# Performance work log

Measured on AMD Instinct MI355X. Metric: run time of the kernel, lower is better.

## Reference

```python
import jax, jax.numpy as jnp
import numpy as np

B, C, N, M, S = 16384, 256, 128, 20, 3  # batch, controller dim, mem locations, mem vec size, shifts
EMIT = M + 1 + 1 + S + 1  # 26


def setup_inputs() -> dict:
    key = jax.random.key(0)
    k1, k2, k3, k4, k5 = jax.random.split(key, 5)
    controller_output = jax.random.normal(k1, (B, C), dtype=jnp.float32)
    w_t_prev = jax.random.uniform(k2, (B, N), dtype=jnp.float32)
    M_t = jax.random.normal(k3, (B, N, M), dtype=jnp.float32)
    # fc_addr dense params (glorot-ish scale)
    W_addr = jax.random.normal(k4, (C, EMIT), dtype=jnp.float32) * (1.0 / np.sqrt(C))
    b_addr = jax.random.normal(k5, (EMIT,), dtype=jnp.float32) * 0.01
    return {"controller_output": controller_output, "w_t_prev": w_t_prev,
            "M_t": M_t, "W_addr": W_addr, "b_addr": b_addr}


def reference(controller_output, w_t_prev, M_t, W_addr, b_addr):
    # fc_addr: Dense with tanh activation
    fc = jnp.tanh(controller_output @ W_addr + b_addr)  # [B, 26]
    k_t = fc[:, :M]                                      # [B, 20]
    beta_t = jax.nn.softplus(fc[:, M:M + 1])             # [B, 1]
    g_t = jax.nn.sigmoid(fc[:, M + 1:M + 2])             # [B, 1]
    s_t = jax.nn.softmax(fc[:, M + 2:M + 2 + S], axis=-1)  # [B, 3]
    gamma_t = 1.0 + jax.nn.softplus(fc[:, M + 2 + S:])   # [B, 1]

    # content addressing: cosine similarity (no epsilon, as in source)
    dot = jnp.einsum('bm,bnm->bn', k_t, M_t)             # [B, N]
    k_mag = jnp.sqrt(jnp.sum(k_t * k_t, axis=-1, keepdims=True))   # [B, 1]
    m_mag = jnp.sqrt(jnp.sum(M_t * M_t, axis=-1))                  # [B, N]
    w_c_t = jax.nn.softmax(beta_t * dot / (k_mag * m_mag), axis=-1)

    # interpolation
    w_g_t = g_t * w_c_t + (1.0 - g_t) * w_t_prev         # [B, N]

    # circular convolutional shift: w~[j] = sum_i s[i] * w_g[(j - (i - S//2)) % N]
    idx = (jnp.arange(N)[:, None] - (jnp.arange(S)[None, :] - S // 2)) % N  # [N, S]
    w_tilde = jnp.einsum('bns,bs->bn', w_g_t[:, idx], s_t)  # [B, N]

    # sharpening
    w_raised = jnp.power(w_tilde, gamma_t)
    w_t = w_raised / jnp.sum(w_raised, axis=-1, keepdims=True)
    return w_t
```

## Files before the change

kernel.cpp:

```cpp
#include <hip/hip_runtime.h>
#include <math.h>

#define B_    16384
#define C_    256
#define N_    128
#define M_    20
#define S_    3
#define EMIT_ 26

__global__ __launch_bounds__(256, 4) void ntm_wave2_kernel(
    const float* __restrict__ ctrl,
    const float* __restrict__ w_prev,
    const float* __restrict__ Mt,
    const float* __restrict__ W,
    const float* __restrict__ bvec,
    float* __restrict__ out)
{
    const int lane = threadIdx.x & 63;
    const int wid  = threadIdx.x >> 6;
    const int b    = blockIdx.x * 4 + wid;

    __shared__ float c_lds[4][C_];

    const float* M0 = Mt + ((size_t)b * N_ + lane) * M_;
    const float* M1 = M0 + (size_t)64 * M_;
    float4 ma[5], mb[5];
    #pragma unroll
    for (int i = 0; i < 5; ++i) ma[i] = *(const float4*)(M0 + 4 * i);
    #pragma unroll
    for (int i = 0; i < 5; ++i) mb[i] = *(const float4*)(M1 + 4 * i);
    const float wp0 = w_prev[(size_t)b * N_ + lane];
    const float wp1 = w_prev[(size_t)b * N_ + lane + 64];

    const float* crow = ctrl + (size_t)b * C_;
    {
        float4 cv = *(const float4*)(crow + lane * 4);
        *(float4*)&c_lds[wid][lane * 4] = cv;
    }

    const int jr = lane & 31;
    const int j  = (jr < EMIT_) ? jr : (EMIT_ - 1);
    const int q  = lane >> 5;
    const float* cq = &c_lds[wid][q * 128];
    const float* Wq = W + (size_t)(q * 128) * EMIT_ + j;
    float a0 = 0.f, a1 = 0.f;
    #pragma unroll 8
    for (int io = 0; io < 128; io += 2) {
        a0 = fmaf(cq[io],     Wq[(size_t)io * EMIT_],       a0);
        a1 = fmaf(cq[io + 1], Wq[(size_t)(io + 1) * EMIT_], a1);
    }
    float a = a0 + a1;
    a += __shfl_xor(a, 32);
    a = tanhf(a + bvec[j]);

    float fc[EMIT_];
    #pragma unroll
    for (int jj = 0; jj < EMIT_; ++jj) fc[jj] = __shfl(a, jj);

    float ksq = 0.f;
    #pragma unroll
    for (int m = 0; m < M_; ++m) ksq = fmaf(fc[m], fc[m], ksq);

    const float beta  = log1pf(__expf(fc[20]));
    const float g     = 1.f / (1.f + __expf(-fc[21]));
    const float e0 = __expf(fc[22]);
    const float e1 = __expf(fc[23]);
    const float e2 = __expf(fc[24]);
    const float einv = 1.f / (e0 + e1 + e2);
    const float s0 = e0 * einv, s1 = e1 * einv, s2 = e2 * einv;
    const float gamma = 1.f + log1pf(__expf(fc[25]));

    float dot0 = 0.f, msq0 = 0.f, dot1 = 0.f, msq1 = 0.f;
    #pragma unroll
    for (int i = 0; i < 5; ++i) {
        float4 v = ma[i];
        dot0 = fmaf(fc[4*i+0], v.x, dot0);  msq0 = fmaf(v.x, v.x, msq0);
        dot0 = fmaf(fc[4*i+1], v.y, dot0);  msq0 = fmaf(v.y, v.y, msq0);
        dot0 = fmaf(fc[4*i+2], v.z, dot0);  msq0 = fmaf(v.z, v.z, msq0);
        dot0 = fmaf(fc[4*i+3], v.w, dot0);  msq0 = fmaf(v.w, v.w, msq0);
    }
    #pragma unroll
    for (int i = 0; i < 5; ++i) {
        float4 v = mb[i];
        dot1 = fmaf(fc[4*i+0], v.x, dot1);  msq1 = fmaf(v.x, v.x, msq1);
        dot1 = fmaf(fc[4*i+1], v.y, dot1);  msq1 = fmaf(v.y, v.y, msq1);
        dot1 = fmaf(fc[4*i+2], v.z, dot1);  msq1 = fmaf(v.z, v.z, msq1);
        dot1 = fmaf(fc[4*i+3], v.w, dot1);  msq1 = fmaf(v.w, v.w, msq1);
    }
    const float l0 = beta * dot0 / sqrtf(ksq * msq0);
    const float l1 = beta * dot1 / sqrtf(ksq * msq1);

    float mx = fmaxf(l0, l1);
    #pragma unroll
    for (int o = 32; o; o >>= 1) mx = fmaxf(mx, __shfl_xor(mx, o));
    const float p0 = __expf(l0 - mx);
    const float p1 = __expf(l1 - mx);
    float sm = p0 + p1;
    #pragma unroll
    for (int o = 32; o; o >>= 1) sm += __shfl_xor(sm, o);
    const float inv_sm = 1.f / sm;

    const float A  = g * (p0 * inv_sm) + (1.f - g) * wp0;
    const float Bv = g * (p1 * inv_sm) + (1.f - g) * wp1;

    const float Ap  = __shfl(A,  (lane + 1) & 63);
    const float Bp  = __shfl(Bv, (lane + 1) & 63);
    const float Am  = __shfl(A,  (lane + 63) & 63);
    const float Bm  = __shfl(Bv, (lane + 63) & 63);
    const float A0  = __shfl(A, 0);
    const float A63 = __shfl(A, 63);
    const float B0  = __shfl(Bv, 0);
    const float B63 = __shfl(Bv, 63);

    const float np0 = (lane == 63) ? B0  : Ap;
    const float nm0 = (lane == 0)  ? B63 : Am;
    const float np1 = (lane == 63) ? A0  : Bp;
    const float nm1 = (lane == 0)  ? A63 : Bm;

    const float wt0 = np0 * s0 + A  * s1 + nm0 * s2;
    const float wt1 = np1 * s0 + Bv * s1 + nm1 * s2;

    const float wr0 = (wt0 > 0.f) ? __expf(gamma * __logf(wt0)) : 0.f;
    const float wr1 = (wt1 > 0.f) ? __expf(gamma * __logf(wt1)) : 0.f;
    float tot = wr0 + wr1;
    #pragma unroll
    for (int o = 32; o; o >>= 1) tot += __shfl_xor(tot, o);
    const float inv_tot = 1.f / tot;

    float* orow = out + (size_t)b * N_;
    orow[lane]      = wr0 * inv_tot;
    orow[lane + 64] = wr1 * inv_tot;
}

extern "C" void kernel_launch(void* const* d_in, const int* in_sizes, int n_in,
                              void* d_out, int out_size, void* d_ws, size_t ws_size,
                              hipStream_t stream) {
    const float* ctrl   = (const float*)d_in[0];
    const float* w_prev = (const float*)d_in[1];
    const float* Mt     = (const float*)d_in[2];
    const float* W      = (const float*)d_in[3];
    const float* bvec   = (const float*)d_in[4];
    float* out = (float*)d_out;

    ntm_wave2_kernel<<<dim3(B_ / 4), dim3(256), 0, stream>>>(ctrl, w_prev, Mt, W, bvec, out);
}
```

Baseline: 42.80 us.

## Restructure fc_addr matvec: 4-way K split, two outputs per lane, no LDS

The dense controller projection is re-partitioned so each lane computes two adjacent output columns over a 64-element slice of C, with four slices combined by shuffles. The LDS staging of the controller row is removed in favour of direct float4 loads, and W is read as float2. The projection now runs before the memory-matrix loads, and the launch-bounds occupancy hint rises from 4 to 5 blocks. The aim is fewer dependent load/FMA iterations and no LDS round trip, at the cost of redundant ctrl loads per lane and more register pressure from the larger occupancy target.

```diff
diff --git a/kernel.cpp b/kernel.cpp
--- a/kernel.cpp
+++ b/kernel.cpp
@@ -8,7 +8,7 @@
 #define S_    3
 #define EMIT_ 26
 
-__global__ __launch_bounds__(256, 4) void ntm_wave2_kernel(
+__global__ __launch_bounds__(256, 5) void ntm_wave3_kernel(
     const float* __restrict__ ctrl,
     const float* __restrict__ w_prev,
     const float* __restrict__ Mt,
@@ -20,7 +20,24 @@
     const int wid  = threadIdx.x >> 6;
     const int b    = blockIdx.x * 4 + wid;
 
-    __shared__ float c_lds[4][C_];
+    const int jp = lane & 15;
+    const int jq = (jp > 12) ? 12 : jp;
+    const int q  = lane >> 4;
+
+    const float* crow = ctrl + (size_t)b * C_ + q * 64;
+    const float* Wq   = W + (size_t)(q * 64) * EMIT_ + 2 * jq;
+    float a0 = 0.f, a1 = 0.f;
+    #pragma unroll
+    for (int c4 = 0; c4 < 16; ++c4) {
+        const float4 cc = *(const float4*)(crow + c4 * 4);
+        #pragma unroll
+        for (int u = 0; u < 4; ++u) {
+            const float  cv = (&cc.x)[u];
+            const float2 wv = *(const float2*)(Wq + (size_t)(c4 * 4 + u) * EMIT_);
+            a0 = fmaf(cv, wv.x, a0);
+            a1 = fmaf(cv, wv.y, a1);
+        }
+    }
 
     const float* M0 = Mt + ((size_t)b * N_ + lane) * M_;
     const float* M1 = M0 + (size_t)64 * M_;
@@ -32,30 +49,16 @@
     const float wp0 = w_prev[(size_t)b * N_ + lane];
     const float wp1 = w_prev[(size_t)b * N_ + lane + 64];
 
-    const float* crow = ctrl + (size_t)b * C_;
-    {
-        float4 cv = *(const float4*)(crow + lane * 4);
-        *(float4*)&c_lds[wid][lane * 4] = cv;
-    }
-
-    const int jr = lane & 31;
-    const int j  = (jr < EMIT_) ? jr : (EMIT_ - 1);
-    const int q  = lane >> 5;
-    const float* cq = &c_lds[wid][q * 128];
-    const float* Wq = W + (size_t)(q * 128) * EMIT_ + j;
-    float a0 = 0.f, a1 = 0.f;
-    #pragma unroll 8
-    for (int io = 0; io < 128; io += 2) {
-        a0 = fmaf(cq[io],     Wq[(size_t)io * EMIT_],       a0);
-        a1 = fmaf(cq[io + 1], Wq[(size_t)(io + 1) * EMIT_], a1);
-    }
-    float a = a0 + a1;
-    a += __shfl_xor(a, 32);
-    a = tanhf(a + bvec[j]);
+    a0 += __shfl_xor(a0, 16);  a0 += __shfl_xor(a0, 32);
+    a1 += __shfl_xor(a1, 16);  a1 += __shfl_xor(a1, 32);
+    const float2 bb = *(const float2*)(bvec + 2 * jq);
+    a0 = tanhf(a0 + bb.x);
+    a1 = tanhf(a1 + bb.y);
 
     float fc[EMIT_];
     #pragma unroll
-    for (int jj = 0; jj < EMIT_; ++jj) fc[jj] = __shfl(a, jj);
+    for (int j = 0; j < EMIT_; ++j)
+        fc[j] = __shfl((j & 1) ? a1 : a0, j >> 1);
 
     float ksq = 0.f;
     #pragma unroll
@@ -73,7 +76,7 @@
     float dot0 = 0.f, msq0 = 0.f, dot1 = 0.f, msq1 = 0.f;
     #pragma unroll
     for (int i = 0; i < 5; ++i) {
-        float4 v = ma[i];
+        const float4 v = ma[i];
         dot0 = fmaf(fc[4*i+0], v.x, dot0);  msq0 = fmaf(v.x, v.x, msq0);
         dot0 = fmaf(fc[4*i+1], v.y, dot0);  msq0 = fmaf(v.y, v.y, msq0);
         dot0 = fmaf(fc[4*i+2], v.z, dot0);  msq0 = fmaf(v.z, v.z, msq0);
@@ -81,7 +84,7 @@
     }
     #pragma unroll
     for (int i = 0; i < 5; ++i) {
-        float4 v = mb[i];
+        const float4 v = mb[i];
         dot1 = fmaf(fc[4*i+0], v.x, dot1);  msq1 = fmaf(v.x, v.x, msq1);
         dot1 = fmaf(fc[4*i+1], v.y, dot1);  msq1 = fmaf(v.y, v.y, msq1);
         dot1 = fmaf(fc[4*i+2], v.z, dot1);  msq1 = fmaf(v.z, v.z, msq1);
@@ -142,5 +145,5 @@
     const float* bvec   = (const float*)d_in[4];
     float* out = (float*)d_out;
 
-    ntm_wave2_kernel<<<dim3(B_ / 4), dim3(256), 0, stream>>>(ctrl, w_prev, Mt, W, bvec, out);
+    ntm_wave3_kernel<<<dim3(B_ / 4), dim3(256), 0, stream>>>(ctrl, w_prev, Mt, W, bvec, out);
 }
```

After: 59.81 us. 1.4x slower.
